# Kernel optimization log

Hardware: AMD Instinct MI355X
Metric: run time of the kernel (lower is better)

## Reference

```python
import jax, jax.numpy as jnp
import numpy as np

ALPHA = 16
M_FACTORS = [8, 16, 8]
N_FACTORS = [8, 16, 8]


def setup_inputs() -> dict:
    key = jax.random.key(0)
    ks = jax.random.split(key, 9)
    B, S, D = 8, 2048, 1024
    r = 8
    x = jax.random.normal(ks[0], (B, S, D), dtype=jnp.float32)
    W = jax.random.normal(ks[1], (D, D), dtype=jnp.float32) * 0.02
    b = jax.random.normal(ks[2], (D,), dtype=jnp.float32) * 0.02
    # m-cores: (r_prev, m_i, r_next), first rank = 1
    core0 = jax.random.normal(ks[3], (1, 8, r), dtype=jnp.float32) * 0.1
    core1 = jax.random.normal(ks[4], (r, 16, r), dtype=jnp.float32) * 0.1
    core2 = jax.random.normal(ks[5], (r, 8, r), dtype=jnp.float32) * 0.1
    # n-cores: (r_prev, n_i, r_next), last rank = 1
    core3 = jax.random.normal(ks[6], (r, 8, r), dtype=jnp.float32) * 0.1
    core4 = jax.random.normal(ks[7], (r, 16, r), dtype=jnp.float32) * 0.1
    core5 = jax.random.normal(ks[8], (r, 8, 1), dtype=jnp.float32) * 0.1
    return {"x": x, "W": W, "b": b, "core0": core0, "core1": core1,
            "core2": core2, "core3": core3, "core4": core4, "core5": core5}


def tensorized_multiplication(x, m_cores, n_cores, m_factors):
    B, S, _ = x.shape
    # [B, 1, S, m_k, ..., m_1] : input dim split into m_factors, reversed
    tt = x.reshape((B, S) + tuple(m_factors[::-1]))[:, None]
    for core in m_cores:
        # contract trailing m-factor and current rank, new rank at axis 1
        tt = jnp.einsum('br...m,rmp->bp...', tt, core)
    for core in n_cores:
        # expand n-factor at the end, carry rank at axis 1
        tt = jnp.einsum('br...,rnp->bp...n', tt, core)
    # tt: [B, 1, S, n_1, ..., n_k] -> [B, S, prod(n_factors)]
    return tt.reshape(B, S, -1)


def reference(x, W, b, core0, core1, core2, core3, core4, core5):
    z = tensorized_multiplication(x, [core0, core1, core2],
                                  [core3, core4, core5], M_FACTORS)
    base = jnp.einsum('bsd,od->bso', x, W) + b  # nn.Linear: x @ W.T + b
    return base + z * ALPHA
```

## Files before the change

### kernel.cpp

```cpp
#include <hip/hip_runtime.h>
#include <hip/hip_bf16.h>


#define D_DIM 1024
#define BS_ROWS 16384
#define ALPHA_F 16.0f
#define BM 128
#define BN 128
#define BK 32

using bf16   = __bf16;
using bf16x8 = __attribute__((ext_vector_type(8))) __bf16;
using bf16x4 = __attribute__((ext_vector_type(4))) __bf16;
using f32x4  = __attribute__((ext_vector_type(4))) float;

#define GPTR(p) (const __attribute__((address_space(1))) void*)(p)
#define SPTR(p) (__attribute__((address_space(3))) void*)(p)

__global__ void fold_cores_kernel(const float* __restrict__ c0,
                                  const float* __restrict__ c1,
                                  const float* __restrict__ c2,
                                  const float* __restrict__ c3,
                                  const float* __restrict__ c4,
                                  const float* __restrict__ c5,
                                  float* __restrict__ Mmat,
                                  float* __restrict__ Nmat)
{
    __shared__ float tmp[1024];
    const int tid = threadIdx.x;

    for (int e = tid; e < 1024; e += 256) {
        int p2 = e & 7, i2i1 = e >> 3;
        int i1 = i2i1 & 7, i2 = i2i1 >> 3;
        float s = 0.f;
        for (int p1 = 0; p1 < 8; ++p1)
            s += c0[i1 * 8 + p1] * c1[p1 * 128 + i2 * 8 + p2];
        tmp[e] = s;
    }
    __syncthreads();
    for (int e = tid; e < 8192; e += 256) {
        int p3 = e & 7, d = e >> 3;
        int i1 = d & 7, i2 = (d >> 3) & 15, i3 = d >> 7;
        float s = 0.f;
        for (int p2 = 0; p2 < 8; ++p2)
            s += tmp[(i2 * 8 + i1) * 8 + p2] * c2[p2 * 64 + i3 * 8 + p3];
        Mmat[e] = s;
    }
    __syncthreads();
    for (int e = tid; e < 1024; e += 256) {
        int nn = e & 127, p4 = e >> 7;
        int n3 = nn & 7, n2 = nn >> 3;
        float s = 0.f;
        for (int p5 = 0; p5 < 8; ++p5)
            s += c4[p4 * 128 + n2 * 8 + p5] * c5[p5 * 8 + n3];
        tmp[e] = s;
    }
    __syncthreads();
    for (int e = tid; e < 8192; e += 256) {
        int o = e & 1023, r3 = e >> 10;
        int n1 = o >> 7, nn = o & 127;
        float s = 0.f;
        for (int p4 = 0; p4 < 8; ++p4)
            s += c3[r3 * 64 + n1 * 8 + p4] * tmp[p4 * 128 + nn];
        Nmat[e] = s;
    }
}

__global__ void build_weff_kernel(const float* __restrict__ W,
                                  const float* __restrict__ Mmat,
                                  const float* __restrict__ Nmat,
                                  bf16* __restrict__ Weff)
{
    int idx = (blockIdx.x * 256 + threadIdx.x) * 4;
    int o = idx >> 10;
    int d0 = idx & 1023;
    f32x4 w = *(const f32x4*)&W[idx];
    bf16x4 v;
    for (int k = 0; k < 4; ++k) {
        float acc = 0.f;
        for (int r = 0; r < 8; ++r)
            acc += Mmat[(d0 + k) * 8 + r] * Nmat[r * 1024 + o];
        v[k] = (bf16)(w[k] + ALPHA_F * acc);
    }
    *(bf16x4*)&Weff[idx] = v;
}

__global__ void cast_x_kernel(const float* __restrict__ X, bf16* __restrict__ Xb)
{
    int i = (blockIdx.x * 256 + threadIdx.x) * 8;
    f32x4 a = *(const f32x4*)&X[i];
    f32x4 b = *(const f32x4*)&X[i + 4];
    bf16x8 v;
    v[0] = (bf16)a[0]; v[1] = (bf16)a[1]; v[2] = (bf16)a[2]; v[3] = (bf16)a[3];
    v[4] = (bf16)b[0]; v[5] = (bf16)b[1]; v[6] = (bf16)b[2]; v[7] = (bf16)b[3];
    *(bf16x8*)&Xb[i] = v;
}

__global__ __launch_bounds__(256) void gemm_bb_kernel(
    const bf16* __restrict__ Xb,
    const bf16* __restrict__ Weff,
    const float* __restrict__ bias,
    float* __restrict__ Out)
{
    __shared__ __align__(16) bf16 As[BM][BK];
    __shared__ __align__(16) bf16 Bs[BN][BK];

    const int tid  = threadIdx.x;
    const int wave = tid >> 6, lane = tid & 63;
    const int mtile = blockIdx.x, ntile = blockIdx.y;
    const int wr = wave >> 1, wc = wave & 1;
    const int l15 = lane & 15, quad = lane >> 4;

    const int srow = wave * 32 + (lane >> 2);
    const int skof = (lane & 3) * 8;
    const bf16* asrc0 = Xb  + (size_t)(mtile * BM + srow) * D_DIM + skof;
    const bf16* asrc1 = asrc0 + 16 * D_DIM;
    const bf16* bsrc0 = Weff + (size_t)(ntile * BN + srow) * D_DIM + skof;
    const bf16* bsrc1 = bsrc0 + 16 * D_DIM;
    char* abase = (char*)&As[0][0];
    char* bbase = (char*)&Bs[0][0];
    void* adst0 = abase + wave * 2048;
    void* adst1 = abase + wave * 2048 + 1024;
    void* bdst0 = bbase + wave * 2048;
    void* bdst1 = bbase + wave * 2048 + 1024;

    f32x4 acc[4][4];
    for (int i = 0; i < 4; ++i)
        for (int j = 0; j < 4; ++j)
            for (int r = 0; r < 4; ++r) acc[i][j][r] = 0.f;

    for (int kt = 0; kt < D_DIM / BK; ++kt) {
        const int ko = kt * BK;
        __builtin_amdgcn_global_load_lds(GPTR(asrc0 + ko), SPTR(adst0), 16, 0, 0);
        __builtin_amdgcn_global_load_lds(GPTR(asrc1 + ko), SPTR(adst1), 16, 0, 0);
        __builtin_amdgcn_global_load_lds(GPTR(bsrc0 + ko), SPTR(bdst0), 16, 0, 0);
        __builtin_amdgcn_global_load_lds(GPTR(bsrc1 + ko), SPTR(bdst1), 16, 0, 0);

        __syncthreads();

        bf16x8 af[4], bfr[4];
        for (int i = 0; i < 4; ++i)
            af[i] = *(const bf16x8*)&As[wr * 64 + i * 16 + l15][quad * 8];
        for (int j = 0; j < 4; ++j)
            bfr[j] = *(const bf16x8*)&Bs[wc * 64 + j * 16 + l15][quad * 8];
        for (int i = 0; i < 4; ++i)
            for (int j = 0; j < 4; ++j)
                acc[i][j] = __builtin_amdgcn_mfma_f32_16x16x32_bf16(
                    af[i], bfr[j], acc[i][j], 0, 0, 0);

        __syncthreads();
    }

    float bj[4];
    for (int j = 0; j < 4; ++j)
        bj[j] = bias[ntile * BN + wc * 64 + j * 16 + l15];
    for (int i = 0; i < 4; ++i) {
        int row0 = mtile * BM + wr * 64 + i * 16 + quad * 4;
        for (int r = 0; r < 4; ++r) {
            float* orow = Out + (size_t)(row0 + r) * D_DIM + ntile * BN + wc * 64 + l15;
            for (int j = 0; j < 4; ++j)
                orow[j * 16] = acc[i][j][r] + bj[j];
        }
    }
}

__global__ __launch_bounds__(256) void gemm_bias_kernel(
    const float* __restrict__ X,
    const bf16* __restrict__ Weff,
    const float* __restrict__ bias,
    float* __restrict__ Out)
{
    __shared__ __align__(16) bf16 As[BM][BK];
    __shared__ __align__(16) bf16 Bs[BN][BK];

    const int tid  = threadIdx.x;
    const int wave = tid >> 6, lane = tid & 63;
    const int mtile = blockIdx.x, ntile = blockIdx.y;
    const int wr = wave >> 1, wc = wave & 1;
    const int l15 = lane & 15, quad = lane >> 4;

    const int ar = tid >> 1, ah = tid & 1;
    const float* xsrc = X + (size_t)(mtile * BM + ar) * D_DIM + ah * 16;
    bf16* adst = &As[ar][ah * 16];

    const bf16* bsrc0 = Weff + (size_t)(ntile * BN + wave * 32 + (lane >> 2)) * D_DIM
                        + (lane & 3) * 8;
    const bf16* bsrc1 = bsrc0 + 16 * D_DIM;
    char* bbase = (char*)&Bs[0][0];
    void* bdst0 = bbase + wave * 2048;
    void* bdst1 = bbase + wave * 2048 + 1024;

    f32x4 acc[4][4];
    for (int i = 0; i < 4; ++i)
        for (int j = 0; j < 4; ++j)
            for (int r = 0; r < 4; ++r) acc[i][j][r] = 0.f;

    for (int kt = 0; kt < D_DIM / BK; ++kt) {
        __builtin_amdgcn_global_load_lds(GPTR(bsrc0 + kt * BK), SPTR(bdst0), 16, 0, 0);
        __builtin_amdgcn_global_load_lds(GPTR(bsrc1 + kt * BK), SPTR(bdst1), 16, 0, 0);

        const f32x4* xp = (const f32x4*)(xsrc + kt * BK);
        f32x4 f0 = xp[0], f1 = xp[1], f2 = xp[2], f3 = xp[3];
        bf16x8 p0, p1;
        p0[0] = (bf16)f0[0]; p0[1] = (bf16)f0[1]; p0[2] = (bf16)f0[2]; p0[3] = (bf16)f0[3];
        p0[4] = (bf16)f1[0]; p0[5] = (bf16)f1[1]; p0[6] = (bf16)f1[2]; p0[7] = (bf16)f1[3];
        p1[0] = (bf16)f2[0]; p1[1] = (bf16)f2[1]; p1[2] = (bf16)f2[2]; p1[3] = (bf16)f2[3];
        p1[4] = (bf16)f3[0]; p1[5] = (bf16)f3[1]; p1[6] = (bf16)f3[2]; p1[7] = (bf16)f3[3];
        *(bf16x8*)adst = p0;
        *(bf16x8*)(adst + 8) = p1;

        __syncthreads();

        bf16x8 af[4], bfr[4];
        for (int i = 0; i < 4; ++i)
            af[i] = *(const bf16x8*)&As[wr * 64 + i * 16 + l15][quad * 8];
        for (int j = 0; j < 4; ++j)
            bfr[j] = *(const bf16x8*)&Bs[wc * 64 + j * 16 + l15][quad * 8];
        for (int i = 0; i < 4; ++i)
            for (int j = 0; j < 4; ++j)
                acc[i][j] = __builtin_amdgcn_mfma_f32_16x16x32_bf16(
                    af[i], bfr[j], acc[i][j], 0, 0, 0);

        __syncthreads();
    }

    float bj[4];
    for (int j = 0; j < 4; ++j)
        bj[j] = bias[ntile * BN + wc * 64 + j * 16 + l15];
    for (int i = 0; i < 4; ++i) {
        int row0 = mtile * BM + wr * 64 + i * 16 + quad * 4;
        for (int r = 0; r < 4; ++r) {
            float* orow = Out + (size_t)(row0 + r) * D_DIM + ntile * BN + wc * 64 + l15;
            for (int j = 0; j < 4; ++j)
                orow[j * 16] = acc[i][j][r] + bj[j];
        }
    }
}

extern "C" void kernel_launch(void* const* d_in, const int* in_sizes, int n_in,
                              void* d_out, int out_size, void* d_ws, size_t ws_size,
                              hipStream_t stream) {
    const float* x  = (const float*)d_in[0];
    const float* W  = (const float*)d_in[1];
    const float* b  = (const float*)d_in[2];
    const float* c0 = (const float*)d_in[3];
    const float* c1 = (const float*)d_in[4];
    const float* c2 = (const float*)d_in[5];
    const float* c3 = (const float*)d_in[6];
    const float* c4 = (const float*)d_in[7];
    const float* c5 = (const float*)d_in[8];
    float* out = (float*)d_out;

    char* ws = (char*)d_ws;
    bf16*  Weff = (bf16*)ws;
    float* Mmat = (float*)(ws + 2u * 1024u * 1024u);
    float* Nmat = (float*)(ws + 2u * 1024u * 1024u + 32u * 1024u);
    bf16*  Xb   = (bf16*)(ws + 4u * 1024u * 1024u);
    const size_t need = 4u * 1024u * 1024u + (size_t)BS_ROWS * D_DIM * 2u;

    fold_cores_kernel<<<1, 256, 0, stream>>>(c0, c1, c2, c3, c4, c5, Mmat, Nmat);
    build_weff_kernel<<<1024, 256, 0, stream>>>(W, Mmat, Nmat, Weff);

    dim3 grid(BS_ROWS / BM, D_DIM / BN);
    if (ws_size >= need) {
        cast_x_kernel<<<(BS_ROWS * D_DIM) / (256 * 8), 256, 0, stream>>>(x, Xb);
        gemm_bb_kernel<<<grid, 256, 0, stream>>>(Xb, Weff, b, out);
    } else {
        gemm_bias_kernel<<<grid, 256, 0, stream>>>(x, Weff, b, out);
    }
}
```

Before: 191.3 us.

## Fuse core folding into Weff build and swizzle GEMM LDS layout

Replaces the single-block core-folding kernel and separate Weff build with one kernel where each block recomputes the M factor in shared memory and its own N column, then writes one Weff row. This removes a serial one-block kernel and the intermediate Mmat/Nmat buffers at the cost of redundant per-block compute. The GEMM also applies an XOR swizzle on the 16-byte chunks written to and read from LDS to reduce bank conflicts on fragment loads.

```diff
diff --git a/kernel.cpp b/kernel.cpp
--- a/kernel.cpp
+++ b/kernel.cpp
@@ -17,17 +17,17 @@
 #define GPTR(p) (const __attribute__((address_space(1))) void*)(p)
 #define SPTR(p) (__attribute__((address_space(3))) void*)(p)
 
-__global__ void fold_cores_kernel(const float* __restrict__ c0,
-                                  const float* __restrict__ c1,
-                                  const float* __restrict__ c2,
-                                  const float* __restrict__ c3,
-                                  const float* __restrict__ c4,
-                                  const float* __restrict__ c5,
-                                  float* __restrict__ Mmat,
-                                  float* __restrict__ Nmat)
-{
-    __shared__ float tmp[1024];
+__global__ __launch_bounds__(256) void build_weff_fused_kernel(
+    const float* __restrict__ W,
+    const float* __restrict__ c0, const float* __restrict__ c1,
+    const float* __restrict__ c2, const float* __restrict__ c3,
+    const float* __restrict__ c4, const float* __restrict__ c5,
+    bf16* __restrict__ Weff)
+{
+    __shared__ float t2[1024];
+    __shared__ float Msh[8192];
     const int tid = threadIdx.x;
+    const int o = blockIdx.x;
 
     for (int e = tid; e < 1024; e += 256) {
         int p2 = e & 7, i2i1 = e >> 3;
@@ -35,7 +35,7 @@
         float s = 0.f;
         for (int p1 = 0; p1 < 8; ++p1)
             s += c0[i1 * 8 + p1] * c1[p1 * 128 + i2 * 8 + p2];
-        tmp[e] = s;
+        t2[e] = s;
     }
     __syncthreads();
     for (int e = tid; e < 8192; e += 256) {
@@ -43,46 +43,37 @@
         int i1 = d & 7, i2 = (d >> 3) & 15, i3 = d >> 7;
         float s = 0.f;
         for (int p2 = 0; p2 < 8; ++p2)
-            s += tmp[(i2 * 8 + i1) * 8 + p2] * c2[p2 * 64 + i3 * 8 + p3];
-        Mmat[e] = s;
-    }
-    __syncthreads();
-    for (int e = tid; e < 1024; e += 256) {
-        int nn = e & 127, p4 = e >> 7;
-        int n3 = nn & 7, n2 = nn >> 3;
+            s += t2[(i2 * 8 + i1) * 8 + p2] * c2[p2 * 64 + i3 * 8 + p3];
+        Msh[e] = s;
+    }
+
+    int n1 = o >> 7, nn = o & 127, n2 = nn >> 3, n3 = nn & 7;
+    float v[8];
+    for (int p4 = 0; p4 < 8; ++p4) {
         float s = 0.f;
         for (int p5 = 0; p5 < 8; ++p5)
             s += c4[p4 * 128 + n2 * 8 + p5] * c5[p5 * 8 + n3];
-        tmp[e] = s;
+        v[p4] = s;
+    }
+    float ncol[8];
+    for (int r3 = 0; r3 < 8; ++r3) {
+        float s = 0.f;
+        for (int p4 = 0; p4 < 8; ++p4)
+            s += c3[r3 * 64 + n1 * 8 + p4] * v[p4];
+        ncol[r3] = s;
     }
     __syncthreads();
-    for (int e = tid; e < 8192; e += 256) {
-        int o = e & 1023, r3 = e >> 10;
-        int n1 = o >> 7, nn = o & 127;
-        float s = 0.f;
-        for (int p4 = 0; p4 < 8; ++p4)
-            s += c3[r3 * 64 + n1 * 8 + p4] * tmp[p4 * 128 + nn];
-        Nmat[e] = s;
-    }
-}
-
-__global__ void build_weff_kernel(const float* __restrict__ W,
-                                  const float* __restrict__ Mmat,
-                                  const float* __restrict__ Nmat,
-                                  bf16* __restrict__ Weff)
-{
-    int idx = (blockIdx.x * 256 + threadIdx.x) * 4;
-    int o = idx >> 10;
-    int d0 = idx & 1023;
-    f32x4 w = *(const f32x4*)&W[idx];
-    bf16x4 v;
+
+    int d0 = tid * 4;
+    f32x4 w = *(const f32x4*)&W[o * D_DIM + d0];
+    bf16x4 res;
     for (int k = 0; k < 4; ++k) {
         float acc = 0.f;
         for (int r = 0; r < 8; ++r)
-            acc += Mmat[(d0 + k) * 8 + r] * Nmat[r * 1024 + o];
-        v[k] = (bf16)(w[k] + ALPHA_F * acc);
-    }
-    *(bf16x4*)&Weff[idx] = v;
+            acc += Msh[(d0 + k) * 8 + r] * ncol[r];
+        res[k] = (bf16)(w[k] + ALPHA_F * acc);
+    }
+    *(bf16x4*)&Weff[o * D_DIM + d0] = res;
 }
 
 __global__ void cast_x_kernel(const float* __restrict__ X, bf16* __restrict__ Xb)
@@ -112,7 +103,7 @@
     const int l15 = lane & 15, quad = lane >> 4;
 
     const int srow = wave * 32 + (lane >> 2);
-    const int skof = (lane & 3) * 8;
+    const int skof = (((lane & 3) ^ ((lane >> 3) & 3)) * 8);
     const bf16* asrc0 = Xb  + (size_t)(mtile * BM + srow) * D_DIM + skof;
     const bf16* asrc1 = asrc0 + 16 * D_DIM;
     const bf16* bsrc0 = Weff + (size_t)(ntile * BN + srow) * D_DIM + skof;
@@ -124,6 +115,8 @@
     void* bdst0 = bbase + wave * 2048;
     void* bdst1 = bbase + wave * 2048 + 1024;
 
+    const int fchunk = (quad ^ ((l15 >> 1) & 3)) * 8;
+
     f32x4 acc[4][4];
     for (int i = 0; i < 4; ++i)
         for (int j = 0; j < 4; ++j)
@@ -140,9 +133,9 @@
 
         bf16x8 af[4], bfr[4];
         for (int i = 0; i < 4; ++i)
-            af[i] = *(const bf16x8*)&As[wr * 64 + i * 16 + l15][quad * 8];
-        for (int j = 0; j < 4; ++j)
-            bfr[j] = *(const bf16x8*)&Bs[wc * 64 + j * 16 + l15][quad * 8];
+            af[i] = *(const bf16x8*)&As[wr * 64 + i * 16 + l15][fchunk];
+        for (int j = 0; j < 4; ++j)
+            bfr[j] = *(const bf16x8*)&Bs[wc * 64 + j * 16 + l15][fchunk];
         for (int i = 0; i < 4; ++i)
             for (int j = 0; j < 4; ++j)
                 acc[i][j] = __builtin_amdgcn_mfma_f32_16x16x32_bf16(
@@ -252,14 +245,11 @@
     float* out = (float*)d_out;
 
     char* ws = (char*)d_ws;
-    bf16*  Weff = (bf16*)ws;
-    float* Mmat = (float*)(ws + 2u * 1024u * 1024u);
-    float* Nmat = (float*)(ws + 2u * 1024u * 1024u + 32u * 1024u);
-    bf16*  Xb   = (bf16*)(ws + 4u * 1024u * 1024u);
+    bf16* Weff = (bf16*)ws;
+    bf16* Xb   = (bf16*)(ws + 4u * 1024u * 1024u);
     const size_t need = 4u * 1024u * 1024u + (size_t)BS_ROWS * D_DIM * 2u;
 
-    fold_cores_kernel<<<1, 256, 0, stream>>>(c0, c1, c2, c3, c4, c5, Mmat, Nmat);
-    build_weff_kernel<<<1024, 256, 0, stream>>>(W, Mmat, Nmat, Weff);
+    build_weff_fused_kernel<<<D_DIM, 256, 0, stream>>>(W, c0, c1, c2, c3, c4, c5, Weff);
 
     dim3 grid(BS_ROWS / BM, D_DIM / BN);
     if (ws_size >= need) {
```

After: 191.7 us. Within noise of the previous version (+0.2%).
